# Performance work log

Hardware: AMD Instinct MI355X
Metric: run time of the kernel (lower is better)

Reference implementation:

```python
import jax, jax.numpy as jnp
import numpy as np

B = 65536
NREQ = 2097152
NVEH = 1048576
NPAS = 2097152
E = 4194304


def _xavier(key, fi, fo):
    gain = 5.0 / 3.0  # tanh gain
    std = gain * np.sqrt(2.0 / (fi + fo))
    return jax.random.normal(key, (fi, fo), dtype=jnp.float32) * std


def scatter_mean(x, idx, num_segments):
    s = jax.ops.segment_sum(x, idx, num_segments=num_segments)
    c = jax.ops.segment_sum(jnp.ones((x.shape[0], 1), x.dtype), idx, num_segments=num_segments)
    return s / jnp.maximum(c, 1.0)


def setup_inputs() -> dict:
    key = jax.random.key(0)
    ks = jax.random.split(key, 16)
    inp = {
        "requests_x": jax.random.normal(ks[0], (NREQ, 10), dtype=jnp.float32),
        "requests_x_batch": jnp.sort(jax.random.randint(ks[1], (NREQ,), 0, B)),
        "vehicles_x": jax.random.normal(ks[2], (NVEH, 8), dtype=jnp.float32),
        "vehicles_x_batch": jnp.sort(jax.random.randint(ks[3], (NVEH,), 0, B)),
        "passengers_x": jax.random.normal(ks[4], (NPAS, 10), dtype=jnp.float32),
        "veh2pas_receiver_edge_index": jax.random.randint(ks[5], (E,), 0, NPAS),
        "veh2pas_sender_edge_index": jax.random.randint(ks[6], (E,), 0, NVEH),
        "req2veh_receiver_start_index": jax.random.randint(ks[7], (B,), 0, NVEH),
        "W_req": _xavier(ks[8], 10, 16), "b_req": jnp.zeros((16,), jnp.float32),
        "W_veh": _xavier(ks[9], 8, 16), "b_veh": jnp.zeros((16,), jnp.float32),
        "W_pas": _xavier(ks[10], 10, 16), "b_pas": jnp.zeros((16,), jnp.float32),
        "W1": _xavier(ks[11], 64, 64), "b1": jnp.zeros((64,), jnp.float32),
        "W2": _xavier(ks[12], 64, 64), "b2": jnp.zeros((64,), jnp.float32),
        "W3": _xavier(ks[13], 64, 1), "b3": jnp.zeros((1,), jnp.float32),
    }
    return inp


def reference(requests_x, requests_x_batch, vehicles_x, vehicles_x_batch, passengers_x,
              veh2pas_receiver_edge_index, veh2pas_sender_edge_index,
              req2veh_receiver_start_index,
              W_req, b_req, W_veh, b_veh, W_pas, b_pas, W1, b1, W2, b2, W3, b3):
    # per-node-type small MLPs
    req_feat = jnp.tanh(requests_x @ W_req + b_req)            # [NREQ,16]
    req_mean = scatter_mean(req_feat, requests_x_batch, B)      # [B,16]
    veh_feat = jnp.tanh(vehicles_x @ W_veh + b_veh)             # [NVEH,16]
    pas_feat = jnp.tanh(passengers_x @ W_pas + b_pas)           # [NPAS,16]
    # gather passengers along edges, mean-pool onto vehicles
    pas_mean = scatter_mean(pas_feat[veh2pas_receiver_edge_index],
                            veh2pas_sender_edge_index, NVEH)    # [NVEH,16]
    ego_feat = jnp.concatenate([veh_feat, pas_mean], axis=-1)[req2veh_receiver_start_index]  # [B,32]
    veh_mean = scatter_mean(veh_feat, vehicles_x_batch, B)      # [B,16]
    action_feat = jnp.concatenate([req_mean, ego_feat, veh_mean], axis=-1)  # [B,64]
    h = jnp.tanh(action_feat @ W1 + b1)
    h = jnp.tanh(h @ W2 + b2)
    return h @ W3 + b3                                          # [B,1]
```

## Files before the change

kernel.cpp:

```cpp
#include <hip/hip_runtime.h>
#include <cstddef>
#include <cstdint>

#define TPB 256
#define BATCH 65536
#define NREQ 2097152
#define NVEH 1048576
#define NEDGE 4194304
#define CAP 32
#define RANK_NEG ((int)0x80808080)

__device__ __forceinline__ float fast_tanh(float x) {
    float e = __expf(2.0f * x);
    return 1.0f - 2.0f / (e + 1.0f);
}
__device__ __forceinline__ float4 tanh4(float4 v) {
    return make_float4(fast_tanh(v.x), fast_tanh(v.y), fast_tanh(v.z), fast_tanh(v.w));
}

template<int F>
__device__ __forceinline__ void load_row(const float* __restrict__ x, int r, float* xr) {
    if constexpr (F == 10) {
        const float2* p = reinterpret_cast<const float2*>(x + (size_t)r * 10);
        #pragma unroll
        for (int i = 0; i < 5; ++i) { float2 t = p[i]; xr[2*i] = t.x; xr[2*i+1] = t.y; }
    } else {
        const float4* p = reinterpret_cast<const float4*>(x + (size_t)r * 8);
        float4 a = p[0], b = p[1];
        xr[0]=a.x; xr[1]=a.y; xr[2]=a.z; xr[3]=a.w;
        xr[4]=b.x; xr[5]=b.y; xr[6]=b.z; xr[7]=b.w;
    }
}

__global__ __launch_bounds__(TPB) void k_bounds(
    const int* __restrict__ req_batch, const int* __restrict__ veh_batch,
    const int* __restrict__ req2veh,
    int* __restrict__ seg_req, int* __restrict__ seg_veh,
    unsigned* __restrict__ markbits, int* __restrict__ rank, int* __restrict__ cnt)
{
    int t = blockIdx.x * TPB + threadIdx.x;
    int i0 = t * 4;
    {
        int4 c = *reinterpret_cast<const int4*>(req_batch + i0);
        int prev = (i0 == 0) ? -1 : req_batch[i0 - 1];
        int vals[4] = {c.x, c.y, c.z, c.w};
        #pragma unroll
        for (int u = 0; u < 4; ++u) {
            for (int b = prev + 1; b <= vals[u]; ++b) seg_req[b] = i0 + u;
            prev = vals[u];
        }
        if (i0 + 4 == NREQ)
            for (int b = prev + 1; b <= BATCH; ++b) seg_req[b] = NREQ;
    }
    if (i0 < NVEH) {
        int4 c = *reinterpret_cast<const int4*>(veh_batch + i0);
        int prev = (i0 == 0) ? -1 : veh_batch[i0 - 1];
        int vals[4] = {c.x, c.y, c.z, c.w};
        #pragma unroll
        for (int u = 0; u < 4; ++u) {
            for (int b = prev + 1; b <= vals[u]; ++b) seg_veh[b] = i0 + u;
            prev = vals[u];
        }
        if (i0 + 4 == NVEH)
            for (int b = prev + 1; b <= BATCH; ++b) seg_veh[b] = NVEH;
    }
    if (i0 < BATCH) {
        int4 vv = *reinterpret_cast<const int4*>(req2veh + i0);
        int vs[4] = {vv.x, vv.y, vv.z, vv.w};
        #pragma unroll
        for (int u = 0; u < 4; ++u) {
            int v = vs[u];
            atomicOr(&markbits[v >> 5], 1u << (v & 31));
            int old = atomicCAS(&rank[v], RANK_NEG, RANK_NEG + 1);
            if (old == RANK_NEG) rank[v] = atomicAdd(cnt, 1);
        }
    }
}

template<int F>
__device__ __forceinline__ void seg_mean_reg(
    const float* __restrict__ x, const int* __restrict__ seg,
    const float* __restrict__ W, const float* __restrict__ bias,
    float* __restrict__ mean_out, int b, int q)
{
    float4 wq[F];
    #pragma unroll
    for (int i = 0; i < F; ++i)
        wq[i] = *reinterpret_cast<const float4*>(&W[i*16 + q*4]);
    float4 bq = reinterpret_cast<const float4*>(bias)[q];

    int lo = seg[b];
    int hi = seg[b + 1];
    float4 s = make_float4(0.f, 0.f, 0.f, 0.f);

    int r = lo;
    for (; r + 4 <= hi; r += 4) {
        float xr[4][F];
        #pragma unroll
        for (int u = 0; u < 4; ++u) load_row<F>(x, r + u, xr[u]);
        #pragma unroll
        for (int u = 0; u < 4; ++u) {
            float4 acc = bq;
            #pragma unroll
            for (int i = 0; i < F; ++i) {
                acc.x = fmaf(xr[u][i], wq[i].x, acc.x);
                acc.y = fmaf(xr[u][i], wq[i].y, acc.y);
                acc.z = fmaf(xr[u][i], wq[i].z, acc.z);
                acc.w = fmaf(xr[u][i], wq[i].w, acc.w);
            }
            float4 tv = tanh4(acc);
            s.x += tv.x; s.y += tv.y; s.z += tv.z; s.w += tv.w;
        }
    }
    for (; r < hi; ++r) {
        float xr[F];
        load_row<F>(x, r, xr);
        float4 acc = bq;
        #pragma unroll
        for (int i = 0; i < F; ++i) {
            acc.x = fmaf(xr[i], wq[i].x, acc.x);
            acc.y = fmaf(xr[i], wq[i].y, acc.y);
            acc.z = fmaf(xr[i], wq[i].z, acc.z);
            acc.w = fmaf(xr[i], wq[i].w, acc.w);
        }
        float4 tv = tanh4(acc);
        s.x += tv.x; s.y += tv.y; s.z += tv.z; s.w += tv.w;
    }
    float inv = 1.0f / fmaxf((float)(hi - lo), 1.0f);
    float4 o = make_float4(s.x*inv, s.y*inv, s.z*inv, s.w*inv);
    reinterpret_cast<float4*>(mean_out)[(size_t)b*4 + q] = o;
}

#define NB_REQ (BATCH/64)
#define NB_VEH (BATCH/64)
#define NB_P1  (NB_REQ + NB_VEH)
#define NB_EDGE (NEDGE/(TPB*4))

__global__ __launch_bounds__(TPB, 4) void k_mid(
    const float* __restrict__ requests_x, const int* __restrict__ seg_req,
    const float* __restrict__ vehicles_x, const int* __restrict__ seg_veh,
    const float* __restrict__ W_req, const float* __restrict__ b_req,
    const float* __restrict__ W_veh, const float* __restrict__ b_veh,
    float* __restrict__ req_mean, float* __restrict__ veh_mean,
    const int* __restrict__ send, const int* __restrict__ recv,
    const unsigned* __restrict__ markbits, const int* __restrict__ rank,
    int* __restrict__ deg, int* __restrict__ bucket)
{
    int blk = blockIdx.x;
    int tid = threadIdx.x;
    if (blk < NB_REQ) {
        int t = blk * TPB + tid;
        seg_mean_reg<10>(requests_x, seg_req, W_req, b_req, req_mean, t >> 2, t & 3);
    } else if (blk < NB_P1) {
        int t = (blk - NB_REQ) * TPB + tid;
        seg_mean_reg<8>(vehicles_x, seg_veh, W_veh, b_veh, veh_mean, t >> 2, t & 3);
    } else {
        int e4 = (blk - NB_P1) * TPB + tid;
        int4 sv = reinterpret_cast<const int4*>(send)[e4];
        int vv[4] = {sv.x, sv.y, sv.z, sv.w};
        #pragma unroll
        for (int u = 0; u < 4; ++u) {
            int v = vv[u];
            if ((markbits[v >> 5] >> (v & 31)) & 1u) {
                int rk = rank[v];
                int slot = atomicAdd(&deg[rk], 1);
                if (slot < CAP) bucket[(size_t)rk * CAP + slot] = recv[e4 * 4 + u];
            }
        }
    }
}

__global__ __launch_bounds__(TPB, 3) void k_final(
    const float* __restrict__ req_mean, const float* __restrict__ veh_mean,
    const int* __restrict__ rank, const int* __restrict__ deg,
    const int* __restrict__ bucket, const float* __restrict__ pas_x,
    const float* __restrict__ vehicles_x, const int* __restrict__ req2veh,
    const float* __restrict__ W_veh, const float* __restrict__ b_veh,
    const float* __restrict__ W_pas, const float* __restrict__ b_pas,
    const float* __restrict__ W1, const float* __restrict__ b1,
    const float* __restrict__ W2, const float* __restrict__ b2,
    const float* __restrict__ W3, const float* __restrict__ b3,
    float* __restrict__ out)
{
    __shared__ __align__(16) float sW1[4096];
    __shared__ __align__(16) float sW2[4096];
    __shared__ float sW3[64];
    __shared__ float sb1[64];
    __shared__ float sb2[64];

    int tid = threadIdx.x;
    {
        const float4* s1 = reinterpret_cast<const float4*>(W1);
        const float4* s2 = reinterpret_cast<const float4*>(W2);
        float4* d1 = reinterpret_cast<float4*>(sW1);
        float4* d2 = reinterpret_cast<float4*>(sW2);
        for (int i = tid; i < 1024; i += TPB) { d1[i] = s1[i]; d2[i] = s2[i]; }
        if (tid < 64) { sW3[tid] = W3[tid]; sb1[tid] = b1[tid]; sb2[tid] = b2[tid]; }
    }
    __syncthreads();

    int q = tid & 3;
    int b = blockIdx.x * (TPB / 4) + (tid >> 2);
    int lane = tid & 63;
    int lbase = lane & ~3;

    float a[64];
    {
        const float4* rs = reinterpret_cast<const float4*>(req_mean) + (size_t)b*4;
        const float4* vs = reinterpret_cast<const float4*>(veh_mean) + (size_t)b*4;
        #pragma unroll
        for (int j4 = 0; j4 < 4; ++j4) {
            float4 t = rs[j4];
            a[4*j4+0]=t.x; a[4*j4+1]=t.y; a[4*j4+2]=t.z; a[4*j4+3]=t.w;
            float4 u = vs[j4];
            a[48+4*j4+0]=u.x; a[48+4*j4+1]=u.y; a[48+4*j4+2]=u.z; a[48+4*j4+3]=u.w;
        }
    }
    int v = req2veh[b];

    float4 fv;
    {
        float4 wv[8];
        #pragma unroll
        for (int i = 0; i < 8; ++i)
            wv[i] = *reinterpret_cast<const float4*>(&W_veh[i*16 + q*4]);
        float4 bv = reinterpret_cast<const float4*>(b_veh)[q];
        float vx[8];
        load_row<8>(vehicles_x, v, vx);
        float4 acc = bv;
        #pragma unroll
        for (int i = 0; i < 8; ++i) {
            acc.x = fmaf(vx[i], wv[i].x, acc.x); acc.y = fmaf(vx[i], wv[i].y, acc.y);
            acc.z = fmaf(vx[i], wv[i].z, acc.z); acc.w = fmaf(vx[i], wv[i].w, acc.w);
        }
        fv = tanh4(acc);
    }

    float4 fp;
    {
        float4 wp[10];
        #pragma unroll
        for (int i = 0; i < 10; ++i)
            wp[i] = *reinterpret_cast<const float4*>(&W_pas[i*16 + q*4]);
        float4 bp = reinterpret_cast<const float4*>(b_pas)[q];
        int r = rank[v];
        int d = deg[r];
        int n = min(d, CAP);
        const int4* bk4 = reinterpret_cast<const int4*>(bucket + (size_t)r * CAP);
        float4 ps = make_float4(0.f, 0.f, 0.f, 0.f);
        for (int c = 0; c * 4 < n; ++c) {
            int4 idx = bk4[c];
            int pv[4] = {idx.x, idx.y, idx.z, idx.w};
            int m = n - c * 4;
            float px[4][10];
            #pragma unroll
            for (int u = 0; u < 4; ++u)
                if (u < m) load_row<10>(pas_x, pv[u], px[u]);
            #pragma unroll
            for (int u = 0; u < 4; ++u) {
                if (u < m) {
                    float4 acc = bp;
                    #pragma unroll
                    for (int i = 0; i < 10; ++i) {
                        acc.x = fmaf(px[u][i], wp[i].x, acc.x);
                        acc.y = fmaf(px[u][i], wp[i].y, acc.y);
                        acc.z = fmaf(px[u][i], wp[i].z, acc.z);
                        acc.w = fmaf(px[u][i], wp[i].w, acc.w);
                    }
                    float4 t = tanh4(acc);
                    ps.x += t.x; ps.y += t.y; ps.z += t.z; ps.w += t.w;
                }
            }
        }
        float inv = 1.0f / fmaxf((float)d, 1.0f);
        fp = make_float4(ps.x*inv, ps.y*inv, ps.z*inv, ps.w*inv);
    }

    #pragma unroll
    for (int src = 0; src < 4; ++src) {
        a[16+4*src+0] = __shfl(fv.x, lbase+src);
        a[16+4*src+1] = __shfl(fv.y, lbase+src);
        a[16+4*src+2] = __shfl(fv.z, lbase+src);
        a[16+4*src+3] = __shfl(fv.w, lbase+src);
        a[32+4*src+0] = __shfl(fp.x, lbase+src);
        a[32+4*src+1] = __shfl(fp.y, lbase+src);
        a[32+4*src+2] = __shfl(fp.z, lbase+src);
        a[32+4*src+3] = __shfl(fp.w, lbase+src);
    }

    const float4* W1v = reinterpret_cast<const float4*>(sW1);
    const float4* W2v = reinterpret_cast<const float4*>(sW2);

    float hq[16];
    {
        float4 acc[4];
        #pragma unroll
        for (int jj = 0; jj < 4; ++jj)
            acc[jj] = *reinterpret_cast<const float4*>(&sb1[q*16 + jj*4]);
        #pragma unroll
        for (int k = 0; k < 64; ++k) {
            float ak = a[k];
            #pragma unroll
            for (int jj = 0; jj < 4; ++jj) {
                float4 w = W1v[k*16 + q*4 + jj];
                acc[jj].x = fmaf(ak, w.x, acc[jj].x); acc[jj].y = fmaf(ak, w.y, acc[jj].y);
                acc[jj].z = fmaf(ak, w.z, acc[jj].z); acc[jj].w = fmaf(ak, w.w, acc[jj].w);
            }
        }
        #pragma unroll
        for (int jj = 0; jj < 4; ++jj) {
            float4 t = tanh4(acc[jj]);
            hq[4*jj+0]=t.x; hq[4*jj+1]=t.y; hq[4*jj+2]=t.z; hq[4*jj+3]=t.w;
        }
    }
    #pragma unroll
    for (int src = 0; src < 4; ++src)
        #pragma unroll
        for (int jj = 0; jj < 16; ++jj)
            a[src*16 + jj] = __shfl(hq[jj], lbase + src);

    float o;
    {
        float4 acc[4];
        #pragma unroll
        for (int jj = 0; jj < 4; ++jj)
            acc[jj] = *reinterpret_cast<const float4*>(&sb2[q*16 + jj*4]);
        #pragma unroll
        for (int k = 0; k < 64; ++k) {
            float ak = a[k];
            #pragma unroll
            for (int jj = 0; jj < 4; ++jj) {
                float4 w = W2v[k*16 + q*4 + jj];
                acc[jj].x = fmaf(ak, w.x, acc[jj].x); acc[jj].y = fmaf(ak, w.y, acc[jj].y);
                acc[jj].z = fmaf(ak, w.z, acc[jj].z); acc[jj].w = fmaf(ak, w.w, acc[jj].w);
            }
        }
        o = 0.0f;
        #pragma unroll
        for (int jj = 0; jj < 4; ++jj) {
            float4 t = tanh4(acc[jj]);
            o = fmaf(t.x, sW3[q*16+4*jj+0], o);
            o = fmaf(t.y, sW3[q*16+4*jj+1], o);
            o = fmaf(t.z, sW3[q*16+4*jj+2], o);
            o = fmaf(t.w, sW3[q*16+4*jj+3], o);
        }
    }
    o += __shfl_xor(o, 1);
    o += __shfl_xor(o, 2);
    if (q == 0) out[b] = o + b3[0];
}

extern "C" void kernel_launch(void* const* d_in, const int* in_sizes, int n_in,
                              void* d_out, int out_size, void* d_ws, size_t ws_size,
                              hipStream_t stream) {
    const float* requests_x = (const float*)d_in[0];
    const int*   req_batch  = (const int*)d_in[1];
    const float* vehicles_x = (const float*)d_in[2];
    const int*   veh_batch  = (const int*)d_in[3];
    const float* pas_x      = (const float*)d_in[4];
    const int*   recv       = (const int*)d_in[5];
    const int*   send       = (const int*)d_in[6];
    const int*   req2veh    = (const int*)d_in[7];
    const float* W_req = (const float*)d_in[8];
    const float* b_req = (const float*)d_in[9];
    const float* W_veh = (const float*)d_in[10];
    const float* b_veh = (const float*)d_in[11];
    const float* W_pas = (const float*)d_in[12];
    const float* b_pas = (const float*)d_in[13];
    const float* W1 = (const float*)d_in[14];
    const float* b1 = (const float*)d_in[15];
    const float* W2 = (const float*)d_in[16];
    const float* b2 = (const float*)d_in[17];
    const float* W3 = (const float*)d_in[18];
    const float* b3 = (const float*)d_in[19];
    float* out = (float*)d_out;

    char* ws = (char*)d_ws;
    float*    req_mean = (float*)   (ws + 0);
    float*    veh_mean = (float*)   (ws + (4u<<20));
    int*      seg_req  = (int*)     (ws + (8u<<20));
    int*      seg_veh  = (int*)     (ws + (9u<<20));
    unsigned* markbits = (unsigned*)(ws + (10u<<20));
    int*      deg      = (int*)     (ws + (10u<<20) + (128u<<10));
    int*      cnt      = (int*)     (ws + (10u<<20) + (384u<<10));
    int*      rank     = (int*)     (ws + (11u<<20));
    int*      bucket   = (int*)     (ws + (15u<<20));

    hipMemsetAsync(markbits, 0, (384u<<10) + 64, stream);
    hipMemsetAsync(rank, 0x80, NVEH * sizeof(int), stream);

    k_bounds<<<NREQ/4/TPB, TPB, 0, stream>>>(
        req_batch, veh_batch, req2veh, seg_req, seg_veh, markbits, rank, cnt);

    k_mid<<<NB_P1 + NB_EDGE, TPB, 0, stream>>>(
        requests_x, seg_req, vehicles_x, seg_veh,
        W_req, b_req, W_veh, b_veh, req_mean, veh_mean,
        send, recv, markbits, rank, deg, bucket);

    k_final<<<BATCH*4/TPB, TPB, 0, stream>>>(
        req_mean, veh_mean, rank, deg, bucket, pas_x,
        vehicles_x, req2veh, W_veh, b_veh, W_pas, b_pas,
        W1, b1, W2, b2, W3, b3, out);
}
```

Baseline: 165.8 us.

## Stage segment rows in LDS and reduce segment means with shared atomics

The per-segment mean phase for requests and vehicles now has each block cover 64 segments. The block copies contiguous row tiles into LDS with coalesced loads, and each 4-thread team processes 4 rows, flushing run sums into shared accumulators with LDS atomics. The old scheme gave one team per segment and read rows from global memory with uneven per-segment loop lengths. The rank sentinel also changes from 0x80 fill to zero with a +1 offset, so one memset clears markbits, deg, cnt and rank together. The cost is extra syncthreads, LDS atomic contention, and reading the batch arrays again.

```diff
diff --git a/kernel.cpp b/kernel.cpp
--- a/kernel.cpp
+++ b/kernel.cpp
@@ -8,7 +8,9 @@
 #define NVEH 1048576
 #define NEDGE 4194304
 #define CAP 32
-#define RANK_NEG ((int)0x80808080)
+#define SPB 64
+#define TILE 256
+#define CH 4
 
 __device__ __forceinline__ float fast_tanh(float x) {
     float e = __expf(2.0f * x);
@@ -19,7 +21,7 @@
 }
 
 template<int F>
-__device__ __forceinline__ void load_row(const float* __restrict__ x, int r, float* xr) {
+__device__ __forceinline__ void load_row_g(const float* __restrict__ x, int r, float* xr) {
     if constexpr (F == 10) {
         const float2* p = reinterpret_cast<const float2*>(x + (size_t)r * 10);
         #pragma unroll
@@ -71,74 +73,106 @@
         for (int u = 0; u < 4; ++u) {
             int v = vs[u];
             atomicOr(&markbits[v >> 5], 1u << (v & 31));
-            int old = atomicCAS(&rank[v], RANK_NEG, RANK_NEG + 1);
-            if (old == RANK_NEG) rank[v] = atomicAdd(cnt, 1);
+            int old = atomicCAS(&rank[v], 0, -1);
+            if (old == 0) rank[v] = 1 + atomicAdd(cnt, 1);
         }
     }
 }
 
 template<int F>
-__device__ __forceinline__ void seg_mean_reg(
-    const float* __restrict__ x, const int* __restrict__ seg,
+__device__ __forceinline__ void phase1_lds(
+    const float* __restrict__ x, const int* __restrict__ batch,
+    const int* __restrict__ seg,
     const float* __restrict__ W, const float* __restrict__ bias,
-    float* __restrict__ mean_out, int b, int q)
+    float* __restrict__ mean_out, int b0,
+    float2* sX, int* sB, float* sAcc, int tid)
 {
+    constexpr int FP2 = F / 2;
+    int team = tid >> 2, q = tid & 3;
+    for (int i = tid; i < SPB * 17; i += TPB) sAcc[i] = 0.0f;
+
     float4 wq[F];
     #pragma unroll
     for (int i = 0; i < F; ++i)
-        wq[i] = *reinterpret_cast<const float4*>(&W[i*16 + q*4]);
+        wq[i] = *reinterpret_cast<const float4*>(&W[i * 16 + q * 4]);
     float4 bq = reinterpret_cast<const float4*>(bias)[q];
 
-    int lo = seg[b];
-    int hi = seg[b + 1];
-    float4 s = make_float4(0.f, 0.f, 0.f, 0.f);
-
-    int r = lo;
-    for (; r + 4 <= hi; r += 4) {
-        float xr[4][F];
-        #pragma unroll
-        for (int u = 0; u < 4; ++u) load_row<F>(x, r + u, xr[u]);
-        #pragma unroll
-        for (int u = 0; u < 4; ++u) {
-            float4 acc = bq;
+    int R0 = seg[b0], R1 = seg[b0 + SPB];
+
+    for (int tb = R0; tb < R1; tb += TILE) {
+        int nr = min(TILE, R1 - tb);
+        __syncthreads();
+        {
+            const float2* src = reinterpret_cast<const float2*>(x + (size_t)tb * F);
+            if constexpr (F == 10) {
+                for (int idx = tid; idx < nr * 5; idx += TPB) sX[idx] = src[idx];
+            } else {
+                for (int idx = tid; idx < nr * 4; idx += TPB)
+                    sX[(idx >> 2) * 5 + (idx & 3)] = src[idx];
+            }
+            for (int idx = tid; idx < nr; idx += TPB) sB[idx] = batch[tb + idx];
+        }
+        __syncthreads();
+
+        int r0 = team * CH;
+        int r1 = min(r0 + CH, nr);
+        int cur = -1;
+        float4 acc = make_float4(0.f, 0.f, 0.f, 0.f);
+        for (int rr = r0; rr < r1; ++rr) {
+            const float2* row = &sX[rr * 5];
+            float xr[F];
+            #pragma unroll
+            for (int i = 0; i < FP2; ++i) {
+                float2 t = row[i];
+                xr[2*i] = t.x; xr[2*i+1] = t.y;
+            }
+            float4 a2 = bq;
             #pragma unroll
             for (int i = 0; i < F; ++i) {
-                acc.x = fmaf(xr[u][i], wq[i].x, acc.x);
-                acc.y = fmaf(xr[u][i], wq[i].y, acc.y);
-                acc.z = fmaf(xr[u][i], wq[i].z, acc.z);
-                acc.w = fmaf(xr[u][i], wq[i].w, acc.w);
-            }
-            float4 tv = tanh4(acc);
-            s.x += tv.x; s.y += tv.y; s.z += tv.z; s.w += tv.w;
-        }
-    }
-    for (; r < hi; ++r) {
-        float xr[F];
-        load_row<F>(x, r, xr);
-        float4 acc = bq;
-        #pragma unroll
-        for (int i = 0; i < F; ++i) {
-            acc.x = fmaf(xr[i], wq[i].x, acc.x);
-            acc.y = fmaf(xr[i], wq[i].y, acc.y);
-            acc.z = fmaf(xr[i], wq[i].z, acc.z);
-            acc.w = fmaf(xr[i], wq[i].w, acc.w);
-        }
-        float4 tv = tanh4(acc);
-        s.x += tv.x; s.y += tv.y; s.z += tv.z; s.w += tv.w;
-    }
-    float inv = 1.0f / fmaxf((float)(hi - lo), 1.0f);
-    float4 o = make_float4(s.x*inv, s.y*inv, s.z*inv, s.w*inv);
-    reinterpret_cast<float4*>(mean_out)[(size_t)b*4 + q] = o;
-}
-
-#define NB_REQ (BATCH/64)
-#define NB_VEH (BATCH/64)
-#define NB_P1  (NB_REQ + NB_VEH)
-#define NB_EDGE (NEDGE/(TPB*4))
+                a2.x = fmaf(xr[i], wq[i].x, a2.x);
+                a2.y = fmaf(xr[i], wq[i].y, a2.y);
+                a2.z = fmaf(xr[i], wq[i].z, a2.z);
+                a2.w = fmaf(xr[i], wq[i].w, a2.w);
+            }
+            float4 tv = tanh4(a2);
+            int s = sB[rr] - b0;
+            if (s != cur) {
+                if (cur >= 0) {
+                    atomicAdd(&sAcc[cur*17 + q*4 + 0], acc.x);
+                    atomicAdd(&sAcc[cur*17 + q*4 + 1], acc.y);
+                    atomicAdd(&sAcc[cur*17 + q*4 + 2], acc.z);
+                    atomicAdd(&sAcc[cur*17 + q*4 + 3], acc.w);
+                }
+                cur = s; acc = tv;
+            } else {
+                acc.x += tv.x; acc.y += tv.y; acc.z += tv.z; acc.w += tv.w;
+            }
+        }
+        if (cur >= 0) {
+            atomicAdd(&sAcc[cur*17 + q*4 + 0], acc.x);
+            atomicAdd(&sAcc[cur*17 + q*4 + 1], acc.y);
+            atomicAdd(&sAcc[cur*17 + q*4 + 2], acc.z);
+            atomicAdd(&sAcc[cur*17 + q*4 + 3], acc.w);
+        }
+    }
+    __syncthreads();
+    for (int idx = tid; idx < SPB * 16; idx += TPB) {
+        int s = idx >> 4;
+        int lo = seg[b0 + s], hi = seg[b0 + s + 1];
+        float inv = 1.0f / fmaxf((float)(hi - lo), 1.0f);
+        mean_out[(size_t)b0 * 16 + idx] = sAcc[s * 17 + (idx & 15)] * inv;
+    }
+}
+
+#define NB_REQ (BATCH / SPB)
+#define NB_P1  (2 * NB_REQ)
+#define NB_EDGE (NEDGE / (TPB * 4))
 
 __global__ __launch_bounds__(TPB, 4) void k_mid(
-    const float* __restrict__ requests_x, const int* __restrict__ seg_req,
-    const float* __restrict__ vehicles_x, const int* __restrict__ seg_veh,
+    const float* __restrict__ requests_x, const int* __restrict__ req_batch,
+    const int* __restrict__ seg_req,
+    const float* __restrict__ vehicles_x, const int* __restrict__ veh_batch,
+    const int* __restrict__ seg_veh,
     const float* __restrict__ W_req, const float* __restrict__ b_req,
     const float* __restrict__ W_veh, const float* __restrict__ b_veh,
     float* __restrict__ req_mean, float* __restrict__ veh_mean,
@@ -146,14 +180,16 @@
     const unsigned* __restrict__ markbits, const int* __restrict__ rank,
     int* __restrict__ deg, int* __restrict__ bucket)
 {
-    int blk = blockIdx.x;
-    int tid = threadIdx.x;
+    __shared__ __align__(16) float2 sX[TILE * 5];
+    __shared__ int   sB[TILE];
+    __shared__ float sAcc[SPB * 17];
+    int blk = blockIdx.x, tid = threadIdx.x;
     if (blk < NB_REQ) {
-        int t = blk * TPB + tid;
-        seg_mean_reg<10>(requests_x, seg_req, W_req, b_req, req_mean, t >> 2, t & 3);
+        phase1_lds<10>(requests_x, req_batch, seg_req, W_req, b_req,
+                       req_mean, blk * SPB, sX, sB, sAcc, tid);
     } else if (blk < NB_P1) {
-        int t = (blk - NB_REQ) * TPB + tid;
-        seg_mean_reg<8>(vehicles_x, seg_veh, W_veh, b_veh, veh_mean, t >> 2, t & 3);
+        phase1_lds<8>(vehicles_x, veh_batch, seg_veh, W_veh, b_veh,
+                      veh_mean, (blk - NB_REQ) * SPB, sX, sB, sAcc, tid);
     } else {
         int e4 = (blk - NB_P1) * TPB + tid;
         int4 sv = reinterpret_cast<const int4*>(send)[e4];
@@ -162,7 +198,7 @@
         for (int u = 0; u < 4; ++u) {
             int v = vv[u];
             if ((markbits[v >> 5] >> (v & 31)) & 1u) {
-                int rk = rank[v];
+                int rk = rank[v] - 1;
                 int slot = atomicAdd(&deg[rk], 1);
                 if (slot < CAP) bucket[(size_t)rk * CAP + slot] = recv[e4 * 4 + u];
             }
@@ -226,7 +262,7 @@
             wv[i] = *reinterpret_cast<const float4*>(&W_veh[i*16 + q*4]);
         float4 bv = reinterpret_cast<const float4*>(b_veh)[q];
         float vx[8];
-        load_row<8>(vehicles_x, v, vx);
+        load_row_g<8>(vehicles_x, v, vx);
         float4 acc = bv;
         #pragma unroll
         for (int i = 0; i < 8; ++i) {
@@ -243,10 +279,10 @@
         for (int i = 0; i < 10; ++i)
             wp[i] = *reinterpret_cast<const float4*>(&W_pas[i*16 + q*4]);
         float4 bp = reinterpret_cast<const float4*>(b_pas)[q];
-        int r = rank[v];
-        int d = deg[r];
+        int rk = rank[v] - 1;
+        int d = deg[rk];
         int n = min(d, CAP);
-        const int4* bk4 = reinterpret_cast<const int4*>(bucket + (size_t)r * CAP);
+        const int4* bk4 = reinterpret_cast<const int4*>(bucket + (size_t)rk * CAP);
         float4 ps = make_float4(0.f, 0.f, 0.f, 0.f);
         for (int c = 0; c * 4 < n; ++c) {
             int4 idx = bk4[c];
@@ -255,7 +291,7 @@
             float px[4][10];
             #pragma unroll
             for (int u = 0; u < 4; ++u)
-                if (u < m) load_row<10>(pas_x, pv[u], px[u]);
+                if (u < m) load_row_g<10>(pas_x, pv[u], px[u]);
             #pragma unroll
             for (int u = 0; u < 4; ++u) {
                 if (u < m) {
@@ -383,17 +419,16 @@
     unsigned* markbits = (unsigned*)(ws + (10u<<20));
     int*      deg      = (int*)     (ws + (10u<<20) + (128u<<10));
     int*      cnt      = (int*)     (ws + (10u<<20) + (384u<<10));
-    int*      rank     = (int*)     (ws + (11u<<20));
+    int*      rank     = (int*)     (ws + (10u<<20) + (388u<<10));
     int*      bucket   = (int*)     (ws + (15u<<20));
 
-    hipMemsetAsync(markbits, 0, (384u<<10) + 64, stream);
-    hipMemsetAsync(rank, 0x80, NVEH * sizeof(int), stream);
+    hipMemsetAsync(markbits, 0, (388u<<10) + (4u<<20), stream);
 
     k_bounds<<<NREQ/4/TPB, TPB, 0, stream>>>(
         req_batch, veh_batch, req2veh, seg_req, seg_veh, markbits, rank, cnt);
 
     k_mid<<<NB_P1 + NB_EDGE, TPB, 0, stream>>>(
-        requests_x, seg_req, vehicles_x, seg_veh,
+        requests_x, req_batch, seg_req, vehicles_x, veh_batch, seg_veh,
         W_req, b_req, W_veh, b_veh, req_mean, veh_mean,
         send, recv, markbits, rank, deg, bucket);
 
```

New measurement: 195.7 us. 18.0% more time.

## Use 16-bit rank table, interleave mid-kernel blocks, vectorize paired row loads

Applied to the files above, without the earlier changes.

Replaces the 32-bit rank array plus bitmask lookup with a 16-bit rank table that uses 0xFFFF as the sentinel. The edge pass then needs only one narrow gather per edge, and the rank is assigned from the atomicOr return value instead of a CAS. k_mid interleaves segment-mean blocks with edge blocks in a 1:2 pattern so the two workload types overlap. Its launch bound changes to 2 blocks per CU. Segment-mean loops now load two rows at a time with float4 loads. The risk is that ranks must fit in 16 bits, which holds only while there are at most 65535 distinct vehicles, and occupancy may shift.

```diff
diff --git a/kernel.cpp b/kernel.cpp
--- a/kernel.cpp
+++ b/kernel.cpp
@@ -8,7 +8,7 @@
 #define NVEH 1048576
 #define NEDGE 4194304
 #define CAP 32
-#define RANK_NEG ((int)0x80808080)
+#define RSENT 0xFFFFu
 
 __device__ __forceinline__ float fast_tanh(float x) {
     float e = __expf(2.0f * x);
@@ -16,27 +16,14 @@
 }
 __device__ __forceinline__ float4 tanh4(float4 v) {
     return make_float4(fast_tanh(v.x), fast_tanh(v.y), fast_tanh(v.z), fast_tanh(v.w));
-}
-
-template<int F>
-__device__ __forceinline__ void load_row(const float* __restrict__ x, int r, float* xr) {
-    if constexpr (F == 10) {
-        const float2* p = reinterpret_cast<const float2*>(x + (size_t)r * 10);
-        #pragma unroll
-        for (int i = 0; i < 5; ++i) { float2 t = p[i]; xr[2*i] = t.x; xr[2*i+1] = t.y; }
-    } else {
-        const float4* p = reinterpret_cast<const float4*>(x + (size_t)r * 8);
-        float4 a = p[0], b = p[1];
-        xr[0]=a.x; xr[1]=a.y; xr[2]=a.z; xr[3]=a.w;
-        xr[4]=b.x; xr[5]=b.y; xr[6]=b.z; xr[7]=b.w;
-    }
 }
 
 __global__ __launch_bounds__(TPB) void k_bounds(
     const int* __restrict__ req_batch, const int* __restrict__ veh_batch,
     const int* __restrict__ req2veh,
     int* __restrict__ seg_req, int* __restrict__ seg_veh,
-    unsigned* __restrict__ markbits, int* __restrict__ rank, int* __restrict__ cnt)
+    unsigned* __restrict__ markbits, unsigned short* __restrict__ rank16,
+    int* __restrict__ cnt)
 {
     int t = blockIdx.x * TPB + threadIdx.x;
     int i0 = t * 4;
@@ -70,11 +57,28 @@
         #pragma unroll
         for (int u = 0; u < 4; ++u) {
             int v = vs[u];
-            atomicOr(&markbits[v >> 5], 1u << (v & 31));
-            int old = atomicCAS(&rank[v], RANK_NEG, RANK_NEG + 1);
-            if (old == RANK_NEG) rank[v] = atomicAdd(cnt, 1);
-        }
-    }
+            unsigned bit = 1u << (v & 31);
+            unsigned old = atomicOr(&markbits[v >> 5], bit);
+            if (!(old & bit))
+                rank16[v] = (unsigned short)atomicAdd(cnt, 1);
+        }
+    }
+}
+
+template<int F>
+__device__ __forceinline__ void mlp_acc(
+    const float* xr, const float4* wq, float4 bq, float4& s)
+{
+    float4 a = bq;
+    #pragma unroll
+    for (int i = 0; i < F; ++i) {
+        a.x = fmaf(xr[i], wq[i].x, a.x);
+        a.y = fmaf(xr[i], wq[i].y, a.y);
+        a.z = fmaf(xr[i], wq[i].z, a.z);
+        a.w = fmaf(xr[i], wq[i].w, a.w);
+    }
+    float4 t = tanh4(a);
+    s.x += t.x; s.y += t.y; s.z += t.z; s.w += t.w;
 }
 
 template<int F>
@@ -93,78 +97,86 @@
     int hi = seg[b + 1];
     float4 s = make_float4(0.f, 0.f, 0.f, 0.f);
 
-    int r = lo;
-    for (; r + 4 <= hi; r += 4) {
-        float xr[4][F];
-        #pragma unroll
-        for (int u = 0; u < 4; ++u) load_row<F>(x, r + u, xr[u]);
-        #pragma unroll
-        for (int u = 0; u < 4; ++u) {
-            float4 acc = bq;
-            #pragma unroll
-            for (int i = 0; i < F; ++i) {
-                acc.x = fmaf(xr[u][i], wq[i].x, acc.x);
-                acc.y = fmaf(xr[u][i], wq[i].y, acc.y);
-                acc.z = fmaf(xr[u][i], wq[i].z, acc.z);
-                acc.w = fmaf(xr[u][i], wq[i].w, acc.w);
-            }
-            float4 tv = tanh4(acc);
-            s.x += tv.x; s.y += tv.y; s.z += tv.z; s.w += tv.w;
-        }
-    }
-    for (; r < hi; ++r) {
-        float xr[F];
-        load_row<F>(x, r, xr);
-        float4 acc = bq;
-        #pragma unroll
-        for (int i = 0; i < F; ++i) {
-            acc.x = fmaf(xr[i], wq[i].x, acc.x);
-            acc.y = fmaf(xr[i], wq[i].y, acc.y);
-            acc.z = fmaf(xr[i], wq[i].z, acc.z);
-            acc.w = fmaf(xr[i], wq[i].w, acc.w);
-        }
-        float4 tv = tanh4(acc);
-        s.x += tv.x; s.y += tv.y; s.z += tv.z; s.w += tv.w;
+    if constexpr (F == 10) {
+        int r = lo;
+        if ((r & 1) && r < hi) {
+            const float2* p = reinterpret_cast<const float2*>(x + (size_t)r * 10);
+            float xr[10];
+            #pragma unroll
+            for (int i = 0; i < 5; ++i) { float2 t = p[i]; xr[2*i] = t.x; xr[2*i+1] = t.y; }
+            mlp_acc<10>(xr, wq, bq, s);
+            ++r;
+        }
+        for (; r + 2 <= hi; r += 2) {
+            const float4* p = reinterpret_cast<const float4*>(x + (size_t)r * 10);
+            float4 v0 = p[0], v1 = p[1], v2 = p[2], v3 = p[3], v4 = p[4];
+            float xr0[10] = {v0.x,v0.y,v0.z,v0.w, v1.x,v1.y,v1.z,v1.w, v2.x,v2.y};
+            float xr1[10] = {v2.z,v2.w, v3.x,v3.y,v3.z,v3.w, v4.x,v4.y,v4.z,v4.w};
+            mlp_acc<10>(xr0, wq, bq, s);
+            mlp_acc<10>(xr1, wq, bq, s);
+        }
+        if (r < hi) {
+            const float2* p = reinterpret_cast<const float2*>(x + (size_t)r * 10);
+            float xr[10];
+            #pragma unroll
+            for (int i = 0; i < 5; ++i) { float2 t = p[i]; xr[2*i] = t.x; xr[2*i+1] = t.y; }
+            mlp_acc<10>(xr, wq, bq, s);
+        }
+    } else {
+        int r = lo;
+        for (; r + 2 <= hi; r += 2) {
+            const float4* p = reinterpret_cast<const float4*>(x + (size_t)r * 8);
+            float4 v0 = p[0], v1 = p[1], v2 = p[2], v3 = p[3];
+            float xr0[8] = {v0.x,v0.y,v0.z,v0.w, v1.x,v1.y,v1.z,v1.w};
+            float xr1[8] = {v2.x,v2.y,v2.z,v2.w, v3.x,v3.y,v3.z,v3.w};
+            mlp_acc<8>(xr0, wq, bq, s);
+            mlp_acc<8>(xr1, wq, bq, s);
+        }
+        if (r < hi) {
+            const float4* p = reinterpret_cast<const float4*>(x + (size_t)r * 8);
+            float4 v0 = p[0], v1 = p[1];
+            float xr0[8] = {v0.x,v0.y,v0.z,v0.w, v1.x,v1.y,v1.z,v1.w};
+            mlp_acc<8>(xr0, wq, bq, s);
+        }
     }
     float inv = 1.0f / fmaxf((float)(hi - lo), 1.0f);
     float4 o = make_float4(s.x*inv, s.y*inv, s.z*inv, s.w*inv);
     reinterpret_cast<float4*>(mean_out)[(size_t)b*4 + q] = o;
 }
 
-#define NB_REQ (BATCH/64)
-#define NB_VEH (BATCH/64)
-#define NB_P1  (NB_REQ + NB_VEH)
-#define NB_EDGE (NEDGE/(TPB*4))
-
-__global__ __launch_bounds__(TPB, 4) void k_mid(
+#define NB_MID 6144
+
+__global__ __launch_bounds__(TPB, 2) void k_mid(
     const float* __restrict__ requests_x, const int* __restrict__ seg_req,
     const float* __restrict__ vehicles_x, const int* __restrict__ seg_veh,
     const float* __restrict__ W_req, const float* __restrict__ b_req,
     const float* __restrict__ W_veh, const float* __restrict__ b_veh,
     float* __restrict__ req_mean, float* __restrict__ veh_mean,
     const int* __restrict__ send, const int* __restrict__ recv,
-    const unsigned* __restrict__ markbits, const int* __restrict__ rank,
+    const unsigned short* __restrict__ rank16,
     int* __restrict__ deg, int* __restrict__ bucket)
 {
-    int blk = blockIdx.x;
-    int tid = threadIdx.x;
-    if (blk < NB_REQ) {
-        int t = blk * TPB + tid;
-        seg_mean_reg<10>(requests_x, seg_req, W_req, b_req, req_mean, t >> 2, t & 3);
-    } else if (blk < NB_P1) {
-        int t = (blk - NB_REQ) * TPB + tid;
-        seg_mean_reg<8>(vehicles_x, seg_veh, W_veh, b_veh, veh_mean, t >> 2, t & 3);
+    int blk = blockIdx.x, tid = threadIdx.x;
+    if (blk % 3 == 0) {
+        int p1 = blk / 3;
+        if (p1 < 1024) {
+            int t = p1 * TPB + tid;
+            seg_mean_reg<10>(requests_x, seg_req, W_req, b_req, req_mean, t >> 2, t & 3);
+        } else {
+            int t = (p1 - 1024) * TPB + tid;
+            seg_mean_reg<8>(vehicles_x, seg_veh, W_veh, b_veh, veh_mean, t >> 2, t & 3);
+        }
     } else {
-        int e4 = (blk - NB_P1) * TPB + tid;
+        int eid = blk - blk / 3 - 1;
+        int e4 = eid * TPB + tid;
         int4 sv = reinterpret_cast<const int4*>(send)[e4];
         int vv[4] = {sv.x, sv.y, sv.z, sv.w};
         #pragma unroll
         for (int u = 0; u < 4; ++u) {
-            int v = vv[u];
-            if ((markbits[v >> 5] >> (v & 31)) & 1u) {
-                int rk = rank[v];
-                int slot = atomicAdd(&deg[rk], 1);
-                if (slot < CAP) bucket[(size_t)rk * CAP + slot] = recv[e4 * 4 + u];
+            unsigned r = rank16[vv[u]];
+            if (r != RSENT) {
+                int slot = atomicAdd(&deg[r], 1);
+                if (slot < CAP) bucket[(size_t)r * CAP + slot] = recv[e4 * 4 + u];
             }
         }
     }
@@ -172,7 +184,7 @@
 
 __global__ __launch_bounds__(TPB, 3) void k_final(
     const float* __restrict__ req_mean, const float* __restrict__ veh_mean,
-    const int* __restrict__ rank, const int* __restrict__ deg,
+    const unsigned short* __restrict__ rank16, const int* __restrict__ deg,
     const int* __restrict__ bucket, const float* __restrict__ pas_x,
     const float* __restrict__ vehicles_x, const int* __restrict__ req2veh,
     const float* __restrict__ W_veh, const float* __restrict__ b_veh,
@@ -225,8 +237,9 @@
         for (int i = 0; i < 8; ++i)
             wv[i] = *reinterpret_cast<const float4*>(&W_veh[i*16 + q*4]);
         float4 bv = reinterpret_cast<const float4*>(b_veh)[q];
-        float vx[8];
-        load_row<8>(vehicles_x, v, vx);
+        const float4* vp = reinterpret_cast<const float4*>(vehicles_x + (size_t)v*8);
+        float4 t0 = vp[0], t1 = vp[1];
+        float vx[8] = {t0.x,t0.y,t0.z,t0.w,t1.x,t1.y,t1.z,t1.w};
         float4 acc = bv;
         #pragma unroll
         for (int i = 0; i < 8; ++i) {
@@ -243,10 +256,10 @@
         for (int i = 0; i < 10; ++i)
             wp[i] = *reinterpret_cast<const float4*>(&W_pas[i*16 + q*4]);
         float4 bp = reinterpret_cast<const float4*>(b_pas)[q];
-        int r = rank[v];
-        int d = deg[r];
+        int rk = rank16[v];
+        int d = deg[rk];
         int n = min(d, CAP);
-        const int4* bk4 = reinterpret_cast<const int4*>(bucket + (size_t)r * CAP);
+        const int4* bk4 = reinterpret_cast<const int4*>(bucket + (size_t)rk * CAP);
         float4 ps = make_float4(0.f, 0.f, 0.f, 0.f);
         for (int c = 0; c * 4 < n; ++c) {
             int4 idx = bk4[c];
@@ -254,8 +267,15 @@
             int m = n - c * 4;
             float px[4][10];
             #pragma unroll
-            for (int u = 0; u < 4; ++u)
-                if (u < m) load_row<10>(pas_x, pv[u], px[u]);
+            for (int u = 0; u < 4; ++u) {
+                if (u < m) {
+                    const float2* pp = reinterpret_cast<const float2*>(pas_x + (size_t)pv[u] * 10);
+                    #pragma unroll
+                    for (int i = 0; i < 5; ++i) {
+                        float2 t = pp[i]; px[u][2*i] = t.x; px[u][2*i+1] = t.y;
+                    }
+                }
+            }
             #pragma unroll
             for (int u = 0; u < 4; ++u) {
                 if (u < m) {
@@ -376,29 +396,29 @@
     float* out = (float*)d_out;
 
     char* ws = (char*)d_ws;
-    float*    req_mean = (float*)   (ws + 0);
-    float*    veh_mean = (float*)   (ws + (4u<<20));
-    int*      seg_req  = (int*)     (ws + (8u<<20));
-    int*      seg_veh  = (int*)     (ws + (9u<<20));
-    unsigned* markbits = (unsigned*)(ws + (10u<<20));
-    int*      deg      = (int*)     (ws + (10u<<20) + (128u<<10));
-    int*      cnt      = (int*)     (ws + (10u<<20) + (384u<<10));
-    int*      rank     = (int*)     (ws + (11u<<20));
-    int*      bucket   = (int*)     (ws + (15u<<20));
-
-    hipMemsetAsync(markbits, 0, (384u<<10) + 64, stream);
-    hipMemsetAsync(rank, 0x80, NVEH * sizeof(int), stream);
+    float*          req_mean = (float*)         (ws + 0);
+    float*          veh_mean = (float*)         (ws + (4u<<20));
+    int*            seg_req  = (int*)           (ws + (8u<<20));
+    int*            seg_veh  = (int*)           (ws + (9u<<20));
+    unsigned*       markbits = (unsigned*)      (ws + (10u<<20));
+    int*            deg      = (int*)           (ws + (10u<<20) + (128u<<10));
+    int*            cnt      = (int*)           (ws + (10u<<20) + (384u<<10));
+    unsigned short* rank16   = (unsigned short*)(ws + (11u<<20));
+    int*            bucket   = (int*)           (ws + (13u<<20));
+
+    hipMemsetAsync(markbits, 0, (388u<<10), stream);
+    hipMemsetAsync(rank16, 0xFF, NVEH * sizeof(unsigned short), stream);
 
     k_bounds<<<NREQ/4/TPB, TPB, 0, stream>>>(
-        req_batch, veh_batch, req2veh, seg_req, seg_veh, markbits, rank, cnt);
-
-    k_mid<<<NB_P1 + NB_EDGE, TPB, 0, stream>>>(
+        req_batch, veh_batch, req2veh, seg_req, seg_veh, markbits, rank16, cnt);
+
+    k_mid<<<NB_MID, TPB, 0, stream>>>(
         requests_x, seg_req, vehicles_x, seg_veh,
         W_req, b_req, W_veh, b_veh, req_mean, veh_mean,
-        send, recv, markbits, rank, deg, bucket);
+        send, recv, rank16, deg, bucket);
 
     k_final<<<BATCH*4/TPB, TPB, 0, stream>>>(
-        req_mean, veh_mean, rank, deg, bucket, pas_x,
+        req_mean, veh_mean, rank16, deg, bucket, pas_x,
         vehicles_x, req2veh, W_veh, b_veh, W_pas, b_pas,
         W1, b1, W2, b2, W3, b3, out);
 }
```

Result: faster. 160.3 us (-3.3%).
